# Optimization experiments

Measured on AMD Instinct MI355X. Metric: run time of the kernel, lower is better.

## Reference

```python
import jax, jax.numpy as jnp
import numpy as np

BETA = 0.25
B, N, D = 8, 4096, 256
NUM_CODES = 4096


def setup_inputs() -> dict:
    key = jax.random.key(0)
    kx, kc = jax.random.split(key)
    x = jax.random.normal(kx, (B, N, D), dtype=jnp.float32)
    # matches nn.init.uniform_(weight, -1/dim, 1/dim)
    codebook = jax.random.uniform(kc, (NUM_CODES, D), dtype=jnp.float32,
                                  minval=-1.0 / D, maxval=1.0 / D)
    return {"x": x, "codebook": codebook}


def reference(x, codebook):
    b, n, d = x.shape
    flat = x.reshape(b * n, d)                                   # [BN, D]
    # squared euclidean distances: ||z||^2 - 2 z.e^T + ||e||^2   # [BN, K]
    distances = (jnp.sum(flat * flat, axis=1, keepdims=True)
                 - 2.0 * jnp.einsum('md,kd->mk', flat, codebook)
                 + jnp.sum(codebook * codebook, axis=1)[None, :])
    indices = jnp.argmin(distances, axis=1)                      # [BN]
    z_q = codebook[indices].reshape(b, n, d)                     # [B, N, D]
    # commitment + codebook losses (detach == stop_gradient)
    sg = jax.lax.stop_gradient
    loss = jnp.mean((sg(z_q) - x) ** 2) + BETA * jnp.mean((z_q - sg(x)) ** 2)
    # straight-through estimator
    z_q_st = x + sg(z_q - x)
    return z_q_st, loss, indices.reshape(b, n)
```

## Files before the change

kernel.cpp:

```cpp
#include <hip/hip_runtime.h>

#define MTOT 32768
#define KC   4096
#define DDIM 256
#define BM   128
#define ZELEMS (MTOT * DDIM)
#define THRESH 2.0e-4f
#define WLCAP 8192
#define RGRID 2048

typedef _Float16 half8 __attribute__((ext_vector_type(8)));
typedef float f32x4 __attribute__((ext_vector_type(4)));

__device__ __forceinline__ void gload_lds16(const void* g, void* l) {
  __builtin_amdgcn_global_load_lds(
      (const __attribute__((address_space(1))) void*)g,
      (__attribute__((address_space(3))) void*)l, 16, 0, 0);
}

__device__ __forceinline__ float sqr_rn(float v) { return __fmul_rn(v, v); }

__global__ __launch_bounds__(256) void vq_prep2(const float* __restrict__ x,
                                                const float* __restrict__ cb,
                                                float* __restrict__ S,
                                                float* __restrict__ cnorm,
                                                _Float16* __restrict__ cbsw,
                                                int* __restrict__ wl_count,
                                                double* __restrict__ accum) {
  const int t = threadIdx.x;
  if (blockIdx.x == 0 && t == 0) { *accum = 0.0; *wl_count = 0; }
  const int sub = t >> 4, lane16 = t & 15;
  const int h = lane16 >> 3, j = lane16 & 7;
  const bool isrow = blockIdx.x < 2048;
  const int idx = (isrow ? blockIdx.x : blockIdx.x - 2048) * 16 + sub;
  const float* p = (isrow ? x + (size_t)idx * DDIM : cb + (size_t)idx * DDIM);

  float r = 0.f;
  const float* q = p + h * 128 + j;
#pragma unroll
  for (int i = 0; i < 16; ++i) r = __fadd_rn(r, sqr_rn(q[i * 8]));
  r = __fadd_rn(r, __shfl_xor(r, 1, 64));
  r = __fadd_rn(r, __shfl_xor(r, 2, 64));
  r = __fadd_rn(r, __shfl_xor(r, 4, 64));
  float sv = __fadd_rn(r, __shfl_xor(r, 8, 64));
  if (lane16 == 0) {
    if (isrow) S[idx] = sv; else cnorm[idx] = sv;
  }

  if (!isrow) {
    const int sw = idx & 7;
    _Float16* dst = cbsw + (size_t)idx * DDIM;
#pragma unroll
    for (int c = 0; c < 2; ++c) {
      int jj = lane16 + c * 16;
      float4 a4 = *reinterpret_cast<const float4*>(p + jj * 8);
      float4 b4 = *reinterpret_cast<const float4*>(p + jj * 8 + 4);
      union { half8 v; _Float16 hh[8]; } u;
      u.hh[0] = (_Float16)(a4.x * 256.0f); u.hh[1] = (_Float16)(a4.y * 256.0f);
      u.hh[2] = (_Float16)(a4.z * 256.0f); u.hh[3] = (_Float16)(a4.w * 256.0f);
      u.hh[4] = (_Float16)(b4.x * 256.0f); u.hh[5] = (_Float16)(b4.y * 256.0f);
      u.hh[6] = (_Float16)(b4.z * 256.0f); u.hh[7] = (_Float16)(b4.w * 256.0f);
      *reinterpret_cast<half8*>(dst + ((jj ^ sw) * 8)) = u.v;
    }
  }
}

__global__ __launch_bounds__(512, 2) void vq_score(const float* __restrict__ x,
                                                   const _Float16* __restrict__ cbsw,
                                                   const float* __restrict__ Sarr,
                                                   const float* __restrict__ cnorm,
                                                   int* __restrict__ bestidx,
                                                   int* __restrict__ wl,
                                                   int* __restrict__ wl_count,
                                                   double* __restrict__ accum) {
  __shared__ _Float16 cbt[2][64 * DDIM];
  __shared__ float cn[KC];
  __shared__ float scrV1[4][BM];
  __shared__ float scrV2[4][BM];
  __shared__ int   scrI1[4][BM];
  __shared__ float wred[8];

  const int t = threadIdx.x;
  const int m0 = blockIdx.x * BM;
  const int lane = t & 63, w = t >> 6;
  const int rg = w >> 2, cg = w & 3;
  const int lo = lane & 15, hi = lane >> 4;

#pragma unroll
  for (int j = 0; j < 4; ++j)
    gload_lds16(cbsw + 0 * 16384 + w * 2048 + j * 512 + lane * 8,
                &cbt[0][w * 2048 + j * 512]);
#pragma unroll
  for (int j = 0; j < 4; ++j)
    gload_lds16(cbsw + 1 * 16384 + w * 2048 + j * 512 + lane * 8,
                &cbt[1][w * 2048 + j * 512]);

#pragma unroll
  for (int i = 0; i < 2; ++i) {
    int fi = t + i * 512;
    *reinterpret_cast<float4*>(&cn[fi * 4]) =
        *reinterpret_cast<const float4*>(cnorm + fi * 4);
  }

  half8 a[4][8];
#pragma unroll
  for (int s2 = 0; s2 < 4; ++s2) {
    const float* xr = x + (size_t)(m0 + rg * 64 + s2 * 16 + lo) * DDIM + hi * 8;
#pragma unroll
    for (int s = 0; s < 8; ++s) {
      float4 u0 = *reinterpret_cast<const float4*>(xr + s * 32);
      float4 u1 = *reinterpret_cast<const float4*>(xr + s * 32 + 4);
      union { half8 v; _Float16 h[8]; } uu;
      uu.h[0] = (_Float16)u0.x; uu.h[1] = (_Float16)u0.y;
      uu.h[2] = (_Float16)u0.z; uu.h[3] = (_Float16)u0.w;
      uu.h[4] = (_Float16)u1.x; uu.h[5] = (_Float16)u1.y;
      uu.h[6] = (_Float16)u1.z; uu.h[7] = (_Float16)u1.w;
      a[s2][s] = uu.v;
    }
  }

  const int code_l = cg * 16 + lo;
  const int bswz = (lo & 7) << 3;

  float v1[4][4], v2[4][4]; int i1[4][4];
#pragma unroll
  for (int s2 = 0; s2 < 4; ++s2)
#pragma unroll
    for (int r = 0; r < 4; ++r) { v1[s2][r] = 3.4e38f; v2[s2][r] = 3.4e38f; i1[s2][r] = 0; }

  __syncthreads();

  for (int kt = 0; kt < KC / 64; ++kt) {
    const int cur = kt & 1;
    if (kt < KC / 64 - 1) asm volatile("s_waitcnt vmcnt(4)" ::: "memory");
    else                  asm volatile("s_waitcnt vmcnt(0)" ::: "memory");
    __builtin_amdgcn_s_barrier();

    const float C = cn[kt * 64 + code_l];
    f32x4 acc[4];
#pragma unroll
    for (int s2 = 0; s2 < 4; ++s2) acc[s2] = (f32x4){0.f, 0.f, 0.f, 0.f};
#pragma unroll
    for (int s = 0; s < 8; ++s) {
      half8 b = *reinterpret_cast<half8*>(
          &cbt[cur][(code_l * DDIM + s * 32 + hi * 8) ^ bswz]);
      acc[0] = __builtin_amdgcn_mfma_f32_16x16x32_f16(a[0][s], b, acc[0], 0, 0, 0);
      acc[1] = __builtin_amdgcn_mfma_f32_16x16x32_f16(a[1][s], b, acc[1], 0, 0, 0);
      acc[2] = __builtin_amdgcn_mfma_f32_16x16x32_f16(a[2][s], b, acc[2], 0, 0, 0);
      acc[3] = __builtin_amdgcn_mfma_f32_16x16x32_f16(a[3][s], b, acc[3], 0, 0, 0);
    }
    const int code = kt * 64 + code_l;
#pragma unroll
    for (int s2 = 0; s2 < 4; ++s2) {
#pragma unroll
      for (int r = 0; r < 4; ++r) {
        float sv = fmaf(acc[s2][r], -0.0078125f, C);
        float mx = fmaxf(v1[s2][r], sv);
        v2[s2][r] = fminf(v2[s2][r], mx);
        bool lt = sv < v1[s2][r];
        if (lt) { v1[s2][r] = sv; i1[s2][r] = code; }
      }
    }

    __builtin_amdgcn_s_barrier();
    if (kt < KC / 64 - 2) {
#pragma unroll
      for (int j = 0; j < 4; ++j)
        gload_lds16(cbsw + (size_t)(kt + 2) * 16384 + w * 2048 + j * 512 + lane * 8,
                    &cbt[cur][w * 2048 + j * 512]);
    }
  }

#pragma unroll
  for (int s2 = 0; s2 < 4; ++s2) {
#pragma unroll
    for (int r = 0; r < 4; ++r) {
      float v = v1[s2][r], u = v2[s2][r]; int ii = i1[s2][r];
#pragma unroll
      for (int m = 1; m <= 8; m <<= 1) {
        float ov = __shfl_xor(v, m, 64);
        int   oi = __shfl_xor(ii, m, 64);
        float ou = __shfl_xor(u, m, 64);
        float mx = fmaxf(v, ov);
        u = fminf(fminf(u, ou), mx);
        bool take = (ov < v) || (ov == v && oi < ii);
        if (take) { v = ov; ii = oi; }
      }
      if (lo == 0) {
        int rowl = rg * 64 + s2 * 16 + hi * 4 + r;
        scrV1[cg][rowl] = v;
        scrV2[cg][rowl] = u;
        scrI1[cg][rowl] = ii;
      }
    }
  }
  __syncthreads();

  float part = 0.f;
  if (t < BM) {
    float bv1 = 3.4e38f, bv2 = 3.4e38f; int bi1 = 0x7fffffff;
#pragma unroll
    for (int c = 0; c < 4; ++c) {
      float v = scrV1[c][t];
      float u = scrV2[c][t];
      int  ii = scrI1[c][t];
      float mx = fmaxf(bv1, v);
      bv2 = fminf(fminf(bv2, u), mx);
      if (v < bv1 || (v == bv1 && ii < bi1)) { bv1 = v; bi1 = ii; }
    }
    int row = m0 + t;
    bestidx[row] = bi1;
    float gap = bv2 - bv1;
    if (gap <= THRESH) {
      int pos = atomicAdd(wl_count, 1);
      if (pos >= WLCAP) part = __fadd_rn(Sarr[row], bv1);
      else wl[pos] = row;
    } else {
      part = __fadd_rn(Sarr[row], bv1);
    }
  }
#pragma unroll
  for (int off = 32; off >= 1; off >>= 1) part += __shfl_down(part, off, 64);
  if (lane == 0) wred[w] = part;
  __syncthreads();
  if (t == 0) {
    double s = 0.0;
#pragma unroll
    for (int i = 0; i < 8; ++i) s += (double)wred[i];
    atomicAdd(accum, s);
  }
}

__global__ __launch_bounds__(256) void vq_rescore(const float* __restrict__ x,
                                                  const float* __restrict__ cb,
                                                  const float* __restrict__ Sarr,
                                                  const float* __restrict__ cnorm,
                                                  const int* __restrict__ wl,
                                                  const int* __restrict__ wl_count,
                                                  float* __restrict__ pD,
                                                  int* __restrict__ pI) {
  const int cnt = min(*wl_count, WLCAP);
  if (cnt == 0) return;
  const int ngroups = (cnt + 7) >> 3;
  const int nitems = ngroups * 16;

  __shared__ float xs[8][260];
  __shared__ int rsh[8];
  __shared__ float scrv[8][4];
  __shared__ int   scri[8][4];

  const int t = threadIdx.x;
  const int lane = t & 63, w = t >> 6;

  for (int item = blockIdx.x; item < nitems; item += RGRID) {
    const int g = item >> 4, chunk = item & 15;
    __syncthreads();
    if (t < 8) { int e = g * 8 + t; rsh[t] = wl[(e < cnt) ? e : g * 8]; }
    __syncthreads();
#pragma unroll
    for (int j = 0; j < 2; ++j) {
      int fi = t + j * 256, i = fi >> 6, dq = fi & 63;
      *reinterpret_cast<float4*>(&xs[i][dq * 4]) =
          *reinterpret_cast<const float4*>(x + (size_t)rsh[i] * DDIM + dq * 4);
    }
    __syncthreads();

    const int code = chunk * 256 + t;
    const float* cp = cb + (size_t)code * DDIM;
    const float C = cnorm[code];

    float acc[8][4];
#pragma unroll
    for (int i = 0; i < 8; ++i)
#pragma unroll
      for (int l = 0; l < 4; ++l) acc[i][l] = 0.f;

#pragma unroll 4
    for (int dq = 0; dq < 64; ++dq) {
      float4 cv = *reinterpret_cast<const float4*>(cp + dq * 4);
#pragma unroll
      for (int i = 0; i < 8; ++i) {
        float4 xv = *reinterpret_cast<float4*>(&xs[i][dq * 4]);
        acc[i][0] = __fadd_rn(acc[i][0], __fmul_rn(xv.x, cv.x));
        acc[i][1] = __fadd_rn(acc[i][1], __fmul_rn(xv.y, cv.y));
        acc[i][2] = __fadd_rn(acc[i][2], __fmul_rn(xv.z, cv.z));
        acc[i][3] = __fadd_rn(acc[i][3], __fmul_rn(xv.w, cv.w));
      }
    }

#pragma unroll
    for (int i = 0; i < 8; ++i) {
      float e = __fadd_rn(__fadd_rn(acc[i][0], acc[i][1]),
                          __fadd_rn(acc[i][2], acc[i][3]));
      float Sv = Sarr[rsh[i]];
      float D = __fadd_rn(__fsub_rn(Sv, __fmul_rn(2.0f, e)), C);
      float v = D; int ii = code;
#pragma unroll
      for (int m = 1; m <= 32; m <<= 1) {
        float ov = __shfl_xor(v, m, 64);
        int   oi = __shfl_xor(ii, m, 64);
        if (ov < v || (ov == v && oi < ii)) { v = ov; ii = oi; }
      }
      if (lane == 0) { scrv[i][w] = v; scri[i][w] = ii; }
    }
    __syncthreads();
    if (t < 8) {
      float bv = 3.4e38f; int bi = 0x7fffffff;
#pragma unroll
      for (int c = 0; c < 4; ++c) {
        float v = scrv[t][c]; int ii = scri[t][c];
        if (v < bv || (v == bv && ii < bi)) { bv = v; bi = ii; }
      }
      int rpos = g * 8 + t;
      if (rpos < cnt) { pD[rpos * 16 + chunk] = bv; pI[rpos * 16 + chunk] = bi; }
    }
  }
}

__global__ __launch_bounds__(256) void vq_combine(const int* __restrict__ wl,
                                                  const int* __restrict__ wl_count,
                                                  const float* __restrict__ pD,
                                                  const int* __restrict__ pI,
                                                  int* __restrict__ bestidx,
                                                  double* __restrict__ accum,
                                                  float* __restrict__ out) {
  __shared__ double dred[4];
  const int cnt = min(*wl_count, WLCAP);
  const int t = threadIdx.x;

  double s = 0.0;
  for (int r = t; r < cnt; r += 256) {
    float bv = 3.4e38f; int bi = 0x7fffffff;
#pragma unroll
    for (int c = 0; c < 16; ++c) {
      float v = pD[r * 16 + c]; int ii = pI[r * 16 + c];
      if (v < bv || (v == bv && ii < bi)) { bv = v; bi = ii; }
    }
    bestidx[wl[r]] = bi;
    s += (double)bv;
  }
#pragma unroll
  for (int off = 32; off >= 1; off >>= 1) s += __shfl_down(s, off, 64);
  if ((t & 63) == 0) dred[t >> 6] = s;
  __syncthreads();
  if (t == 0) {
    double tot = (dred[0] + dred[1]) + (dred[2] + dred[3]);
    double prev = atomicAdd(accum, tot);
    out[ZELEMS] = (float)(1.25 * (prev + tot) / (double)ZELEMS);
  }
}

__global__ __launch_bounds__(256) void vq_emit(const float* __restrict__ x,
                                               const float* __restrict__ cb,
                                               const int* __restrict__ bestidx,
                                               float* __restrict__ out) {
  __shared__ int ish[64];
  const int t = threadIdx.x;
  const int m0 = blockIdx.x * 64;
  if (t < 64) {
    int ii = bestidx[m0 + t];
    ish[t] = ii;
    out[(size_t)ZELEMS + 1 + m0 + t] = (float)ii;
  }
  __syncthreads();
#pragma unroll
  for (int i = 0; i < 16; ++i) {
    int fi = t + i * 256;
    int row = fi >> 6, dc = fi & 63;
    int code = ish[row];
    float4 c4 = *reinterpret_cast<const float4*>(cb + (size_t)code * DDIM + dc * 4);
    float4 x4 = *reinterpret_cast<const float4*>(x + (size_t)(m0 + row) * DDIM + dc * 4);
    float4 o;
    o.x = __fadd_rn(x4.x, __fsub_rn(c4.x, x4.x));
    o.y = __fadd_rn(x4.y, __fsub_rn(c4.y, x4.y));
    o.z = __fadd_rn(x4.z, __fsub_rn(c4.z, x4.z));
    o.w = __fadd_rn(x4.w, __fsub_rn(c4.w, x4.w));
    *reinterpret_cast<float4*>(out + (size_t)(m0 + row) * DDIM + dc * 4) = o;
  }
}

extern "C" void kernel_launch(void* const* d_in, const int* in_sizes, int n_in,
                              void* d_out, int out_size, void* d_ws, size_t ws_size,
                              hipStream_t stream) {
  const float* x  = (const float*)d_in[0];
  const float* cb = (const float*)d_in[1];
  float* out = (float*)d_out;

  char* ws = (char*)d_ws;
  float*     S        = (float*)(ws + 0);
  float*     cnorm    = (float*)(ws + 131072);
  int*       bestidx  = (int*)  (ws + 147456);
  int*       wl       = (int*)  (ws + 278528);
  int*       wl_count = (int*)  (ws + 311296);
  double*    accum    = (double*)(ws + 311312);
  float*     pD       = (float*)(ws + 315392);
  int*       pI       = (int*)  (ws + 839680);
  _Float16*  cbsw     = (_Float16*)(ws + 1363968);

  vq_prep2<<<2304, 256, 0, stream>>>(x, cb, S, cnorm, cbsw, wl_count, accum);
  vq_score<<<MTOT / BM, 512, 0, stream>>>(x, cbsw, S, cnorm, bestidx, wl, wl_count, accum);
  vq_rescore<<<RGRID, 256, 0, stream>>>(x, cb, S, cnorm, wl, wl_count, pD, pI);
  vq_combine<<<1, 256, 0, stream>>>(wl, wl_count, pD, pI, bestidx, accum, out);
  vq_emit<<<MTOT / 64, 256, 0, stream>>>(x, cb, bestidx, out);
}
```

Baseline: 164.2 us.

## Fuse row-norm computation into score kernel and triple-buffer codebook tiles

Row squared norms move out of the prep kernel and into the score kernel, which already reads the x rows, so prep only handles the codebook and re-reading x in a separate pass is avoided. The LDS codebook staging grows from two to three buffers, so the prefetch for tile kt+2 is issued right after the top barrier and the second barrier per iteration is dropped. The second-best tracking uses a single fmed3 instead of max+min. The extra 32KB of LDS may reduce occupancy below the requested two blocks per CU.

```diff
diff --git a/kernel.cpp b/kernel.cpp
--- a/kernel.cpp
+++ b/kernel.cpp
@@ -20,20 +20,17 @@
 
 __device__ __forceinline__ float sqr_rn(float v) { return __fmul_rn(v, v); }
 
-__global__ __launch_bounds__(256) void vq_prep2(const float* __restrict__ x,
-                                                const float* __restrict__ cb,
-                                                float* __restrict__ S,
-                                                float* __restrict__ cnorm,
-                                                _Float16* __restrict__ cbsw,
-                                                int* __restrict__ wl_count,
-                                                double* __restrict__ accum) {
+__global__ __launch_bounds__(256) void vq_prepcb(const float* __restrict__ cb,
+                                                 float* __restrict__ cnorm,
+                                                 _Float16* __restrict__ cbsw,
+                                                 int* __restrict__ wl_count,
+                                                 double* __restrict__ accum) {
   const int t = threadIdx.x;
   if (blockIdx.x == 0 && t == 0) { *accum = 0.0; *wl_count = 0; }
   const int sub = t >> 4, lane16 = t & 15;
   const int h = lane16 >> 3, j = lane16 & 7;
-  const bool isrow = blockIdx.x < 2048;
-  const int idx = (isrow ? blockIdx.x : blockIdx.x - 2048) * 16 + sub;
-  const float* p = (isrow ? x + (size_t)idx * DDIM : cb + (size_t)idx * DDIM);
+  const int idx = blockIdx.x * 16 + sub;
+  const float* p = cb + (size_t)idx * DDIM;
 
   float r = 0.f;
   const float* q = p + h * 128 + j;
@@ -43,38 +40,35 @@
   r = __fadd_rn(r, __shfl_xor(r, 2, 64));
   r = __fadd_rn(r, __shfl_xor(r, 4, 64));
   float sv = __fadd_rn(r, __shfl_xor(r, 8, 64));
-  if (lane16 == 0) {
-    if (isrow) S[idx] = sv; else cnorm[idx] = sv;
-  }
-
-  if (!isrow) {
-    const int sw = idx & 7;
-    _Float16* dst = cbsw + (size_t)idx * DDIM;
-#pragma unroll
-    for (int c = 0; c < 2; ++c) {
-      int jj = lane16 + c * 16;
-      float4 a4 = *reinterpret_cast<const float4*>(p + jj * 8);
-      float4 b4 = *reinterpret_cast<const float4*>(p + jj * 8 + 4);
-      union { half8 v; _Float16 hh[8]; } u;
-      u.hh[0] = (_Float16)(a4.x * 256.0f); u.hh[1] = (_Float16)(a4.y * 256.0f);
-      u.hh[2] = (_Float16)(a4.z * 256.0f); u.hh[3] = (_Float16)(a4.w * 256.0f);
-      u.hh[4] = (_Float16)(b4.x * 256.0f); u.hh[5] = (_Float16)(b4.y * 256.0f);
-      u.hh[6] = (_Float16)(b4.z * 256.0f); u.hh[7] = (_Float16)(b4.w * 256.0f);
-      *reinterpret_cast<half8*>(dst + ((jj ^ sw) * 8)) = u.v;
-    }
+  if (lane16 == 0) cnorm[idx] = sv;
+
+  const int sw = idx & 7;
+  _Float16* dst = cbsw + (size_t)idx * DDIM;
+#pragma unroll
+  for (int c = 0; c < 2; ++c) {
+    int jj = lane16 + c * 16;
+    float4 a4 = *reinterpret_cast<const float4*>(p + jj * 8);
+    float4 b4 = *reinterpret_cast<const float4*>(p + jj * 8 + 4);
+    union { half8 v; _Float16 hh[8]; } u;
+    u.hh[0] = (_Float16)(a4.x * 256.0f); u.hh[1] = (_Float16)(a4.y * 256.0f);
+    u.hh[2] = (_Float16)(a4.z * 256.0f); u.hh[3] = (_Float16)(a4.w * 256.0f);
+    u.hh[4] = (_Float16)(b4.x * 256.0f); u.hh[5] = (_Float16)(b4.y * 256.0f);
+    u.hh[6] = (_Float16)(b4.z * 256.0f); u.hh[7] = (_Float16)(b4.w * 256.0f);
+    *reinterpret_cast<half8*>(dst + ((jj ^ sw) * 8)) = u.v;
   }
 }
 
 __global__ __launch_bounds__(512, 2) void vq_score(const float* __restrict__ x,
                                                    const _Float16* __restrict__ cbsw,
-                                                   const float* __restrict__ Sarr,
+                                                   float* __restrict__ Sarr,
                                                    const float* __restrict__ cnorm,
                                                    int* __restrict__ bestidx,
                                                    int* __restrict__ wl,
                                                    int* __restrict__ wl_count,
                                                    double* __restrict__ accum) {
-  __shared__ _Float16 cbt[2][64 * DDIM];
+  __shared__ _Float16 cbt[3][64 * DDIM];
   __shared__ float cn[KC];
+  __shared__ float sS[BM];
   __shared__ float scrV1[4][BM];
   __shared__ float scrV2[4][BM];
   __shared__ int   scrI1[4][BM];
@@ -119,6 +113,24 @@
     }
   }
 
+  {
+    const int sub = t >> 4, lane16 = t & 15;
+    const int h = lane16 >> 3, jj = lane16 & 7;
+#pragma unroll
+    for (int p = 0; p < 4; ++p) {
+      int rowl = p * 32 + sub;
+      const float* q = x + (size_t)(m0 + rowl) * DDIM + h * 128 + jj;
+      float r = 0.f;
+#pragma unroll
+      for (int i = 0; i < 16; ++i) r = __fadd_rn(r, sqr_rn(q[i * 8]));
+      r = __fadd_rn(r, __shfl_xor(r, 1, 64));
+      r = __fadd_rn(r, __shfl_xor(r, 2, 64));
+      r = __fadd_rn(r, __shfl_xor(r, 4, 64));
+      float sv = __fadd_rn(r, __shfl_xor(r, 8, 64));
+      if (lane16 == 0) { sS[rowl] = sv; Sarr[m0 + rowl] = sv; }
+    }
+  }
+
   const int code_l = cg * 16 + lo;
   const int bswz = (lo & 7) << 3;
 
@@ -130,11 +142,19 @@
 
   __syncthreads();
 
+  int cur = 0;
   for (int kt = 0; kt < KC / 64; ++kt) {
-    const int cur = kt & 1;
     if (kt < KC / 64 - 1) asm volatile("s_waitcnt vmcnt(4)" ::: "memory");
     else                  asm volatile("s_waitcnt vmcnt(0)" ::: "memory");
     __builtin_amdgcn_s_barrier();
+
+    if (kt < KC / 64 - 2) {
+      int stg = cur + 2; if (stg >= 3) stg -= 3;
+#pragma unroll
+      for (int j = 0; j < 4; ++j)
+        gload_lds16(cbsw + (size_t)(kt + 2) * 16384 + w * 2048 + j * 512 + lane * 8,
+                    &cbt[stg][w * 2048 + j * 512]);
+    }
 
     const float C = cn[kt * 64 + code_l];
     f32x4 acc[4];
@@ -155,20 +175,12 @@
 #pragma unroll
       for (int r = 0; r < 4; ++r) {
         float sv = fmaf(acc[s2][r], -0.0078125f, C);
-        float mx = fmaxf(v1[s2][r], sv);
-        v2[s2][r] = fminf(v2[s2][r], mx);
+        v2[s2][r] = __builtin_amdgcn_fmed3f(sv, v1[s2][r], v2[s2][r]);
         bool lt = sv < v1[s2][r];
         if (lt) { v1[s2][r] = sv; i1[s2][r] = code; }
       }
     }
-
-    __builtin_amdgcn_s_barrier();
-    if (kt < KC / 64 - 2) {
-#pragma unroll
-      for (int j = 0; j < 4; ++j)
-        gload_lds16(cbsw + (size_t)(kt + 2) * 16384 + w * 2048 + j * 512 + lane * 8,
-                    &cbt[cur][w * 2048 + j * 512]);
-    }
+    cur = (cur == 2) ? 0 : cur + 1;
   }
 
 #pragma unroll
@@ -213,10 +225,10 @@
     float gap = bv2 - bv1;
     if (gap <= THRESH) {
       int pos = atomicAdd(wl_count, 1);
-      if (pos >= WLCAP) part = __fadd_rn(Sarr[row], bv1);
+      if (pos >= WLCAP) part = __fadd_rn(sS[t], bv1);
       else wl[pos] = row;
     } else {
-      part = __fadd_rn(Sarr[row], bv1);
+      part = __fadd_rn(sS[t], bv1);
     }
   }
 #pragma unroll
@@ -397,7 +409,7 @@
   int*       pI       = (int*)  (ws + 839680);
   _Float16*  cbsw     = (_Float16*)(ws + 1363968);
 
-  vq_prep2<<<2304, 256, 0, stream>>>(x, cb, S, cnorm, cbsw, wl_count, accum);
+  vq_prepcb<<<KC / 16, 256, 0, stream>>>(cb, cnorm, cbsw, wl_count, accum);
   vq_score<<<MTOT / BM, 512, 0, stream>>>(x, cbsw, S, cnorm, bestidx, wl, wl_count, accum);
   vq_rescore<<<RGRID, 256, 0, stream>>>(x, cb, S, cnorm, wl, wl_count, pD, pI);
   vq_combine<<<1, 256, 0, stream>>>(wl, wl_count, pD, pI, bestidx, accum, out);
```

Result: slower. 188.1 us (+14.6%).
